# Kernel optimization log

Measured on AMD Instinct MI355X. Metric: run time of the kernel, lower is better.

Reference implementation:

```python
import jax, jax.numpy as jnp
import numpy as np

B, N, QDIM = 2, 4096, 768
H, D = 8, 64  # num_head, head_dim; inner_dim = 512
INNER = H * D


def setup_inputs() -> dict:
    key = jax.random.key(0)
    ks = jax.random.split(key, 6)
    s = lambda fan_in: 1.0 / np.sqrt(fan_in)
    return {
        "x": jax.random.normal(ks[0], (B, N, QDIM), dtype=jnp.float32),
        "Wq": jax.random.normal(ks[1], (QDIM, INNER), dtype=jnp.float32) * s(QDIM),
        "Wk": jax.random.normal(ks[2], (QDIM, INNER), dtype=jnp.float32) * s(QDIM),
        "Wv": jax.random.normal(ks[3], (QDIM, INNER), dtype=jnp.float32) * s(QDIM),
        "Wout": jax.random.normal(ks[4], (INNER, QDIM), dtype=jnp.float32) * s(INNER),
        "b_out": jnp.zeros((QDIM,), dtype=jnp.float32),
    }


def reference(x, Wq, Wk, Wv, Wout, b_out):
    # x: [b, n, q_dim]; self-attention (kv = x), no mask, dropout = 0 (eval).
    scale = D ** -0.5
    # project and split heads: [b, n, h*d] -> [b, h, n, d]
    def heads(t):
        b, n, _ = t.shape
        return t.reshape(b, n, H, D).transpose(0, 2, 1, 3)
    q = heads(x @ Wq)
    k = heads(x @ Wk)
    v = heads(x @ Wv)
    qk = jnp.einsum("bhid,bhjd->bhij", q, k) * scale  # [b, h, n, n] -- O(n^2) matrix
    attn = jax.nn.softmax(qk, axis=-1)
    out = jnp.einsum("bhij,bhjd->bhid", attn, v)  # [b, h, n, d]
    out = out.transpose(0, 2, 1, 3).reshape(x.shape[0], x.shape[1], INNER)
    return out @ Wout + b_out
```

## Files before the change

kernel.cpp:

```cpp
#include <hip/hip_runtime.h>
#include <cstdint>
#include <cstddef>


typedef __attribute__((ext_vector_type(8))) short short8;
typedef __attribute__((ext_vector_type(4))) float f32x4;

__device__ __forceinline__ unsigned short f2bf(float f) {
  unsigned int u = __float_as_uint(f);
  u = (u + 0x7fffu + ((u >> 16) & 1u)) >> 16;
  return (unsigned short)u;
}

__device__ __forceinline__ float fast_exp2(float x) {
#if __has_builtin(__builtin_amdgcn_exp2f)
  return __builtin_amdgcn_exp2f(x);
#else
  return __expf(x * 0.69314718055994531f);
#endif
}

__device__ __forceinline__ void gld16(const void* g, void* l) {
  __builtin_amdgcn_global_load_lds(
      (__attribute__((address_space(1))) void*)const_cast<void*>(g),
      (__attribute__((address_space(3))) void*)l, 16, 0, 0);
}


__global__ __launch_bounds__(256) void cvt_x_k(const float* __restrict__ x,
                                               unsigned short* __restrict__ xb) {
  const size_t i = ((size_t)blockIdx.x * 256 + threadIdx.x) * 4;
  const float4 v = *(const float4*)(x + i);
  ushort4 u;
  u.x = f2bf(v.x); u.y = f2bf(v.y); u.z = f2bf(v.z); u.w = f2bf(v.w);
  *(ushort4*)(xb + i) = u;
}

__global__ __launch_bounds__(256) void transpose_qkv_w(
    const float* __restrict__ Wq, const float* __restrict__ Wk,
    const float* __restrict__ Wv, unsigned short* __restrict__ Wt) {
  const int id = blockIdx.x * 256 + threadIdx.x;
  const int k = id / 512, n = id % 512;
  const float* W = (blockIdx.y == 0) ? Wq : (blockIdx.y == 1) ? Wk : Wv;
  Wt[(size_t)blockIdx.y * 393216 + (size_t)n * 768 + k] = f2bf(W[id]);
}

__global__ __launch_bounds__(256) void transpose_wout_k(
    const float* __restrict__ Wout, unsigned short* __restrict__ WoT) {
  const int id = blockIdx.x * 256 + threadIdx.x;
  const int k = id / 768, n = id % 768;
  WoT[(size_t)n * 512 + k] = f2bf(Wout[id]);
}


__global__ __launch_bounds__(256) void gemm_qkv_k(
    const unsigned short* __restrict__ A,
    const unsigned short* __restrict__ Wt,
    unsigned short* __restrict__ qb, unsigned short* __restrict__ kb,
    unsigned short* __restrict__ vtb) {
  __shared__ __align__(16) short Al[4096];
  __shared__ __align__(16) short Bl[4096];
  const int tid = threadIdx.x;
  const int w = tid >> 6, lane = tid & 63, quad = lane >> 4, l15 = lane & 15;
  const int wy = w >> 1, wx = w & 1;
  const int m0 = blockIdx.x * 128, n0 = blockIdx.y * 128;
  const unsigned short* Bt = Wt + (size_t)blockIdx.z * (512 * 768);

  f32x4 acc[4][4];
#pragma unroll
  for (int i = 0; i < 4; ++i)
#pragma unroll
    for (int j = 0; j < 4; ++j) acc[i][j] = (f32x4){0.f, 0.f, 0.f, 0.f};

  for (int k0 = 0; k0 < 768; k0 += 32) {
    __syncthreads();
#pragma unroll
    for (int s = 0; s < 2; ++s) {
      const int t = s * 256 + tid;
      gld16(A + (size_t)(m0 + (t >> 2)) * 768 + k0 + (t & 3) * 8,
            Al + s * 2048 + w * 512);
      gld16(Bt + (size_t)(n0 + (t >> 2)) * 768 + k0 + (t & 3) * 8,
            Bl + s * 2048 + w * 512);
    }
    __syncthreads();
    short8 af[4], bf[4];
#pragma unroll
    for (int i = 0; i < 4; ++i) {
      af[i] = *(const short8*)(Al + (wy * 64 + i * 16 + l15) * 32 + quad * 8);
      bf[i] = *(const short8*)(Bl + (wx * 64 + i * 16 + l15) * 32 + quad * 8);
    }
#pragma unroll
    for (int i = 0; i < 4; ++i)
#pragma unroll
      for (int j = 0; j < 4; ++j)
        acc[i][j] = __builtin_amdgcn_mfma_f32_16x16x32_bf16(af[i], bf[j], acc[i][j], 0, 0, 0);
  }

  const int z = blockIdx.z;
#pragma unroll
  for (int i = 0; i < 4; ++i) {
#pragma unroll
    for (int j = 0; j < 4; ++j) {
#pragma unroll
      for (int r = 0; r < 4; ++r) {
        const int m = m0 + wy * 64 + i * 16 + quad * 4 + r;
        const int col = n0 + wx * 64 + j * 16 + l15;
        const int b = m >> 12, nseq = m & 4095;
        const int h = col >> 6, d = col & 63;
        const int bh = b * 8 + h;
        if (z == 0) {
          qb[(size_t)(bh * 4096 + nseq) * 64 + d] =
              f2bf(acc[i][j][r] * 0.18033688011112042f);
        } else if (z == 1) {
          kb[(size_t)(bh * 4096 + nseq) * 64 + d] = f2bf(acc[i][j][r]);
        } else {
          vtb[(size_t)(bh * 64 + d) * 4096 + nseq] = f2bf(acc[i][j][r]);
        }
      }
    }
  }
}


__global__ __launch_bounds__(256) void attn_k(
    const unsigned short* __restrict__ qb,
    const unsigned short* __restrict__ kb,
    const unsigned short* __restrict__ vtb,
    unsigned short* __restrict__ ob) {
  __shared__ __align__(16) short Kl[2][64][32];
  __shared__ __align__(16) short Vl[2][64][32];
  __shared__ __align__(16) short Pl[4][2048];
  const int tid = threadIdx.x;
  const int w = tid >> 6, lane = tid & 63, quad = lane >> 4, l15 = lane & 15;
  const int bh = blockIdx.y;
  const int q0 = blockIdx.x * 128;
  const unsigned short* qbase = qb + (size_t)bh * 4096 * 64;
  const unsigned short* kbase = kb + (size_t)bh * 4096 * 64;
  const unsigned short* vbase = vtb + (size_t)bh * 64 * 4096;
  short* pw = &Pl[w][0];

  short8 qf[2][2];
#pragma unroll
  for (int qh = 0; qh < 2; ++qh) {
    const int qrow = q0 + w * 32 + qh * 16 + l15;
    qf[qh][0] = *(const short8*)(qbase + (size_t)qrow * 64 + quad * 8);
    qf[qh][1] = *(const short8*)(qbase + (size_t)qrow * 64 + 32 + quad * 8);
  }

  const short one_bf = (short)0x3F80;
  const short8 vones = {one_bf, one_bf, one_bf, one_bf,
                        one_bf, one_bf, one_bf, one_bf};

  f32x4 Oacc[2][4];
#pragma unroll
  for (int qh = 0; qh < 2; ++qh)
#pragma unroll
    for (int nf = 0; nf < 4; ++nf) Oacc[qh][nf] = (f32x4){0.f, 0.f, 0.f, 0.f};
  f32x4 Lacc[2] = {(f32x4){0.f, 0.f, 0.f, 0.f}, (f32x4){0.f, 0.f, 0.f, 0.f}};

  const int k2x16 = ((l15 >> 2) & 3) * 16;
  for (int j0 = 0; j0 < 4096; j0 += 64) {
    __syncthreads();
#pragma unroll
    for (int c = 0; c < 2; ++c) {
      gld16(kbase + (size_t)(j0 + (tid >> 2)) * 64 + c * 32 + (tid & 3) * 8,
            &Kl[c][w * 16][0]);
      gld16(vbase + (size_t)(tid >> 2) * 4096 + j0 + c * 32 + (tid & 3) * 8,
            &Vl[c][w * 16][0]);
    }
    __syncthreads();

    f32x4 S[2][4];
#pragma unroll
    for (int nf = 0; nf < 4; ++nf) {
      const short8 b0 = *(const short8*)&Kl[0][nf * 16 + l15][quad * 8];
      const short8 b1 = *(const short8*)&Kl[1][nf * 16 + l15][quad * 8];
#pragma unroll
      for (int qh = 0; qh < 2; ++qh) {
        f32x4 s = (f32x4){0.f, 0.f, 0.f, 0.f};
        s = __builtin_amdgcn_mfma_f32_16x16x32_bf16(qf[qh][0], b0, s, 0, 0, 0);
        s = __builtin_amdgcn_mfma_f32_16x16x32_bf16(qf[qh][1], b1, s, 0, 0, 0);
        S[qh][nf] = s;
      }
    }

#pragma unroll
    for (int qh = 0; qh < 2; ++qh)
#pragma unroll
      for (int nf = 0; nf < 4; ++nf)
#pragma unroll
        for (int r = 0; r < 4; ++r) {
          const float p = fast_exp2(S[qh][nf][r]);
          pw[(qh * 16 + quad * 4 + r) * 64 + ((nf * 16 + l15) ^ (quad * 16))] =
              (short)(__float_as_uint(p) >> 16);
        }

    asm volatile("s_waitcnt lgkmcnt(0)" ::: "memory");

#pragma unroll
    for (int c = 0; c < 2; ++c) {
      short8 pa[2];
#pragma unroll
      for (int qh = 0; qh < 2; ++qh)
        pa[qh] = *(const short8*)(pw + (qh * 16 + l15) * 64 +
                                  ((c * 32 + quad * 8) ^ k2x16));
#pragma unroll
      for (int nf = 0; nf < 4; ++nf) {
        const short8 vb = *(const short8*)&Vl[c][nf * 16 + l15][quad * 8];
#pragma unroll
        for (int qh = 0; qh < 2; ++qh)
          Oacc[qh][nf] =
              __builtin_amdgcn_mfma_f32_16x16x32_bf16(pa[qh], vb, Oacc[qh][nf], 0, 0, 0);
      }
#pragma unroll
      for (int qh = 0; qh < 2; ++qh)
        Lacc[qh] = __builtin_amdgcn_mfma_f32_16x16x32_bf16(pa[qh], vones, Lacc[qh], 0, 0, 0);
    }
  }

  const int b = bh >> 3, h = bh & 7;
#pragma unroll
  for (int qh = 0; qh < 2; ++qh) {
#pragma unroll
    for (int r = 0; r < 4; ++r) {
      const float inv = 1.0f / Lacc[qh][r];
      const int row = q0 + w * 32 + qh * 16 + quad * 4 + r;
#pragma unroll
      for (int nf = 0; nf < 4; ++nf)
        ob[(size_t)(b * 4096 + row) * 512 + h * 64 + nf * 16 + l15] =
            f2bf(Oacc[qh][nf][r] * inv);
    }
  }
}


__global__ __launch_bounds__(256) void gemm_out_k(
    const unsigned short* __restrict__ A,
    const unsigned short* __restrict__ Bt,
    const float* __restrict__ bias, float* __restrict__ out) {
  __shared__ __align__(16) short Al[4096];
  __shared__ __align__(16) short Bl[4096];
  const int tid = threadIdx.x;
  const int w = tid >> 6, lane = tid & 63, quad = lane >> 4, l15 = lane & 15;
  const int wy = w >> 1, wx = w & 1;
  const int m0 = blockIdx.x * 128, n0 = blockIdx.y * 128;

  f32x4 acc[4][4];
#pragma unroll
  for (int i = 0; i < 4; ++i)
#pragma unroll
    for (int j = 0; j < 4; ++j) acc[i][j] = (f32x4){0.f, 0.f, 0.f, 0.f};

  for (int k0 = 0; k0 < 512; k0 += 32) {
    __syncthreads();
#pragma unroll
    for (int s = 0; s < 2; ++s) {
      const int t = s * 256 + tid;
      gld16(A + (size_t)(m0 + (t >> 2)) * 512 + k0 + (t & 3) * 8,
            Al + s * 2048 + w * 512);
      gld16(Bt + (size_t)(n0 + (t >> 2)) * 512 + k0 + (t & 3) * 8,
            Bl + s * 2048 + w * 512);
    }
    __syncthreads();
    short8 af[4], bf[4];
#pragma unroll
    for (int i = 0; i < 4; ++i) {
      af[i] = *(const short8*)(Al + (wy * 64 + i * 16 + l15) * 32 + quad * 8);
      bf[i] = *(const short8*)(Bl + (wx * 64 + i * 16 + l15) * 32 + quad * 8);
    }
#pragma unroll
    for (int i = 0; i < 4; ++i)
#pragma unroll
      for (int j = 0; j < 4; ++j)
        acc[i][j] = __builtin_amdgcn_mfma_f32_16x16x32_bf16(af[i], bf[j], acc[i][j], 0, 0, 0);
  }

#pragma unroll
  for (int i = 0; i < 4; ++i) {
#pragma unroll
    for (int j = 0; j < 4; ++j) {
#pragma unroll
      for (int r = 0; r < 4; ++r) {
        const int m = m0 + wy * 64 + i * 16 + quad * 4 + r;
        const int col = n0 + wx * 64 + j * 16 + l15;
        out[(size_t)m * 768 + col] = acc[i][j][r] + bias[col];
      }
    }
  }
}


extern "C" void kernel_launch(void* const* d_in, const int* in_sizes, int n_in,
                              void* d_out, int out_size, void* d_ws, size_t ws_size,
                              hipStream_t stream) {
  const float* x    = (const float*)d_in[0];
  const float* Wq   = (const float*)d_in[1];
  const float* Wk   = (const float*)d_in[2];
  const float* Wv   = (const float*)d_in[3];
  const float* Wout = (const float*)d_in[4];
  const float* bout = (const float*)d_in[5];
  float* out = (float*)d_out;
  char* ws = (char*)d_ws;

  unsigned short* xb  = (unsigned short*)(ws);
  unsigned short* Wt  = (unsigned short*)(ws + 12582912);
  unsigned short* WoT = (unsigned short*)(ws + 14942208);
  unsigned short* qb  = (unsigned short*)(ws + 15728640);
  unsigned short* kb  = (unsigned short*)(ws + 24117248);
  unsigned short* vtb = (unsigned short*)(ws + 32505856);
  unsigned short* ob  = (unsigned short*)(ws + 40894464);

  cvt_x_k<<<6144, 256, 0, stream>>>(x, xb);
  transpose_qkv_w<<<dim3(1536, 3), 256, 0, stream>>>(Wq, Wk, Wv, Wt);
  transpose_wout_k<<<1536, 256, 0, stream>>>(Wout, WoT);
  gemm_qkv_k<<<dim3(64, 4, 3), 256, 0, stream>>>(xb, Wt, qb, kb, vtb);
  attn_k<<<dim3(32, 16), 256, 0, stream>>>(qb, kb, vtb, ob);
  gemm_out_k<<<dim3(64, 6), 256, 0, stream>>>(ob, WoT, bout, out);
}
```

Before: 260.3 us.

## Load K/V fragments directly to registers in attention; fuse tiled weight transposes

```diff
diff --git a/kernel.cpp b/kernel.cpp
--- a/kernel.cpp
+++ b/kernel.cpp
@@ -36,20 +36,27 @@
   *(ushort4*)(xb + i) = u;
 }
 
-__global__ __launch_bounds__(256) void transpose_qkv_w(
+__global__ __launch_bounds__(256) void transpose_w_k(
     const float* __restrict__ Wq, const float* __restrict__ Wk,
-    const float* __restrict__ Wv, unsigned short* __restrict__ Wt) {
-  const int id = blockIdx.x * 256 + threadIdx.x;
-  const int k = id / 512, n = id % 512;
-  const float* W = (blockIdx.y == 0) ? Wq : (blockIdx.y == 1) ? Wk : Wv;
-  Wt[(size_t)blockIdx.y * 393216 + (size_t)n * 768 + k] = f2bf(W[id]);
-}
-
-__global__ __launch_bounds__(256) void transpose_wout_k(
-    const float* __restrict__ Wout, unsigned short* __restrict__ WoT) {
-  const int id = blockIdx.x * 256 + threadIdx.x;
-  const int k = id / 768, n = id % 768;
-  WoT[(size_t)n * 512 + k] = f2bf(Wout[id]);
+    const float* __restrict__ Wv, const float* __restrict__ Wout,
+    unsigned short* __restrict__ Wt,
+    unsigned short* __restrict__ WoT)
+{
+  __shared__ float t[32][33];
+  const int z = blockIdx.z;
+  const float* src = (z == 0) ? Wq : (z == 1) ? Wk : (z == 2) ? Wv : Wout;
+  const int R = (z < 3) ? 768 : 512, C = (z < 3) ? 512 : 768;
+  unsigned short* dst = (z < 3) ? (Wt + (size_t)z * 393216) : WoT;
+  const int tx = threadIdx.x & 31, ty = threadIdx.x >> 5;
+  const int c0 = blockIdx.x * 32, r0 = blockIdx.y * 32;
+  if (c0 >= C || r0 >= R) return;
+#pragma unroll
+  for (int k = 0; k < 4; ++k)
+    t[ty + 8 * k][tx] = src[(size_t)(r0 + ty + 8 * k) * C + c0 + tx];
+  __syncthreads();
+#pragma unroll
+  for (int k = 0; k < 4; ++k)
+    dst[(size_t)(c0 + ty + 8 * k) * R + r0 + tx] = f2bf(t[tx][ty + 8 * k]);
 }
 
 
@@ -127,8 +134,6 @@
     const unsigned short* __restrict__ kb,
     const unsigned short* __restrict__ vtb,
     unsigned short* __restrict__ ob) {
-  __shared__ __align__(16) short Kl[2][64][32];
-  __shared__ __align__(16) short Vl[2][64][32];
   __shared__ __align__(16) short Pl[4][2048];
   const int tid = threadIdx.x;
   const int w = tid >> 6, lane = tid & 63, quad = lane >> 4, l15 = lane & 15;
@@ -147,6 +152,9 @@
     qf[qh][1] = *(const short8*)(qbase + (size_t)qrow * 64 + 32 + quad * 8);
   }
 
+  const unsigned short* kp = kbase + (size_t)l15 * 64 + quad * 8;
+  const unsigned short* vp = vbase + (size_t)l15 * 4096 + quad * 8;
+
   const short one_bf = (short)0x3F80;
   const short8 vones = {one_bf, one_bf, one_bf, one_bf,
                         one_bf, one_bf, one_bf, one_bf};
@@ -158,31 +166,42 @@
     for (int nf = 0; nf < 4; ++nf) Oacc[qh][nf] = (f32x4){0.f, 0.f, 0.f, 0.f};
   f32x4 Lacc[2] = {(f32x4){0.f, 0.f, 0.f, 0.f}, (f32x4){0.f, 0.f, 0.f, 0.f}};
 
+  short8 kf[8];
+#pragma unroll
+  for (int c = 0; c < 2; ++c)
+#pragma unroll
+    for (int nf = 0; nf < 4; ++nf)
+      kf[c * 4 + nf] = *(const short8*)(kp + (size_t)(nf * 16) * 64 + c * 32);
+
   const int k2x16 = ((l15 >> 2) & 3) * 16;
   for (int j0 = 0; j0 < 4096; j0 += 64) {
-    __syncthreads();
-#pragma unroll
-    for (int c = 0; c < 2; ++c) {
-      gld16(kbase + (size_t)(j0 + (tid >> 2)) * 64 + c * 32 + (tid & 3) * 8,
-            &Kl[c][w * 16][0]);
-      gld16(vbase + (size_t)(tid >> 2) * 4096 + j0 + c * 32 + (tid & 3) * 8,
-            &Vl[c][w * 16][0]);
-    }
-    __syncthreads();
+    short8 vf[8];
+#pragma unroll
+    for (int c = 0; c < 2; ++c)
+#pragma unroll
+      for (int nf = 0; nf < 4; ++nf)
+        vf[c * 4 + nf] =
+            *(const short8*)(vp + (size_t)(nf * 16) * 4096 + j0 + c * 32);
 
     f32x4 S[2][4];
 #pragma unroll
-    for (int nf = 0; nf < 4; ++nf) {
-      const short8 b0 = *(const short8*)&Kl[0][nf * 16 + l15][quad * 8];
-      const short8 b1 = *(const short8*)&Kl[1][nf * 16 + l15][quad * 8];
+    for (int nf = 0; nf < 4; ++nf)
 #pragma unroll
       for (int qh = 0; qh < 2; ++qh) {
         f32x4 s = (f32x4){0.f, 0.f, 0.f, 0.f};
-        s = __builtin_amdgcn_mfma_f32_16x16x32_bf16(qf[qh][0], b0, s, 0, 0, 0);
-        s = __builtin_amdgcn_mfma_f32_16x16x32_bf16(qf[qh][1], b1, s, 0, 0, 0);
+        s = __builtin_amdgcn_mfma_f32_16x16x32_bf16(qf[qh][0], kf[nf], s, 0, 0, 0);
+        s = __builtin_amdgcn_mfma_f32_16x16x32_bf16(qf[qh][1], kf[4 + nf], s, 0, 0, 0);
         S[qh][nf] = s;
       }
-    }
+
+    const int jn = (j0 + 64) & 4095;
+    short8 kn[8];
+#pragma unroll
+    for (int c = 0; c < 2; ++c)
+#pragma unroll
+      for (int nf = 0; nf < 4; ++nf)
+        kn[c * 4 + nf] =
+            *(const short8*)(kp + (size_t)(jn + nf * 16) * 64 + c * 32);
 
 #pragma unroll
     for (int qh = 0; qh < 2; ++qh)
@@ -206,16 +225,18 @@
                                   ((c * 32 + quad * 8) ^ k2x16));
 #pragma unroll
       for (int nf = 0; nf < 4; ++nf) {
-        const short8 vb = *(const short8*)&Vl[c][nf * 16 + l15][quad * 8];
 #pragma unroll
         for (int qh = 0; qh < 2; ++qh)
-          Oacc[qh][nf] =
-              __builtin_amdgcn_mfma_f32_16x16x32_bf16(pa[qh], vb, Oacc[qh][nf], 0, 0, 0);
+          Oacc[qh][nf] = __builtin_amdgcn_mfma_f32_16x16x32_bf16(
+              pa[qh], vf[c * 4 + nf], Oacc[qh][nf], 0, 0, 0);
       }
 #pragma unroll
       for (int qh = 0; qh < 2; ++qh)
         Lacc[qh] = __builtin_amdgcn_mfma_f32_16x16x32_bf16(pa[qh], vones, Lacc[qh], 0, 0, 0);
     }
+
+#pragma unroll
+    for (int i = 0; i < 8; ++i) kf[i] = kn[i];
   }
 
   const int b = bh >> 3, h = bh & 7;
@@ -311,8 +332,7 @@
   unsigned short* ob  = (unsigned short*)(ws + 40894464);
 
   cvt_x_k<<<6144, 256, 0, stream>>>(x, xb);
-  transpose_qkv_w<<<dim3(1536, 3), 256, 0, stream>>>(Wq, Wk, Wv, Wt);
-  transpose_wout_k<<<1536, 256, 0, stream>>>(Wout, WoT);
+  transpose_w_k<<<dim3(24, 24, 4), 256, 0, stream>>>(Wq, Wk, Wv, Wout, Wt, WoT);
   gemm_qkv_k<<<dim3(64, 4, 3), 256, 0, stream>>>(xb, Wt, qb, kb, vtb);
   attn_k<<<dim3(32, 16), 256, 0, stream>>>(qb, kb, vtb, ob);
   gemm_out_k<<<dim3(64, 6), 256, 0, stream>>>(ob, WoT, bout, out);
```

Measured after the change: 374.1 us. 1.44x slower.
